# Optimization experiments

Measured on AMD Instinct MI355X. Metric: run time of the kernel, lower is better.

## Reference

```python
import jax, jax.numpy as jnp
import numpy as np

GRID_MIN = -2.0
GRID_MAX = 2.0
NUM_GRIDS = 8
IN_DIM = 512
OUT_DIM = 512
N = 16384
SPLINE_SCALE = 0.1


def setup_inputs() -> dict:
    key = jax.random.key(0)
    k_x, k_sw, k_w, k_b = jax.random.split(key, 4)
    x = jax.random.normal(k_x, (N, IN_DIM), dtype=jnp.float32)
    grid = jnp.linspace(GRID_MIN, GRID_MAX, NUM_GRIDS, dtype=jnp.float32)
    spline_weight = jax.random.normal(k_sw, (IN_DIM * NUM_GRIDS, OUT_DIM), dtype=jnp.float32) * SPLINE_SCALE
    bound = 1.0 / np.sqrt(IN_DIM)
    base_w = jax.random.uniform(k_w, (OUT_DIM, IN_DIM), minval=-bound, maxval=bound, dtype=jnp.float32)
    base_b = jax.random.uniform(k_b, (OUT_DIM,), minval=-bound, maxval=bound, dtype=jnp.float32)
    return {"x": x, "grid": grid, "spline_weight": spline_weight, "base_w": base_w, "base_b": base_b}


def reference(x, grid, spline_weight, base_w, base_b):
    # Gaussian RBF basis over the grid: (N, in_dim, num_grids)
    h = (GRID_MAX - GRID_MIN) / (NUM_GRIDS - 1)  # grid spacing
    basis = jnp.exp(-(((x[..., None] - grid) / h) ** 2))
    ret = basis.reshape(x.shape[0], -1) @ spline_weight  # (N, out_dim)
    base = jax.nn.silu(x) @ base_w.T + base_b
    return ret + base
```

## Files before the change

kernel.cpp:

```cpp
#include <hip/hip_runtime.h>
#include <hip/hip_bf16.h>

typedef __attribute__((ext_vector_type(8))) short short8;
typedef __attribute__((ext_vector_type(4))) float floatx4;

#define N_ROWS   16384
#define IN_DIM   512
#define OUT_DIM  512
#define K_SPLINE 4096
#define K_TOT    4608
#define NPER     36
#define NSPER    32
#define NKTILE   144
#define ROWS_B   128
#define COLS_B   128
#define L2E      1.4426950408889634f
#define C2E      0.13533528323661270f

__device__ __forceinline__ unsigned short f2bf(float f) {
    unsigned int u = __float_as_uint(f);
    unsigned int r = u + 0x7FFFu + ((u >> 16) & 1u);
    return (unsigned short)(r >> 16);
}

__device__ __forceinline__ unsigned packtrunc(float f0, float f1) {
    return __builtin_amdgcn_perm(__float_as_uint(f1), __float_as_uint(f0), 0x07060302);
}

__global__ __launch_bounds__(256) void prep_kernel(
    const float* __restrict__ sw, const float* __restrict__ bw,
    unsigned short* __restrict__ Btf)
{
    const int t     = threadIdx.x;
    const int lane  = t & 63;
    const int kt32  = blockIdx.x * 4 + (t >> 6);
    const int ct    = blockIdx.y;
    const int mn    = lane & 15, q = lane >> 4;
    const int n     = ct * 16 + mn;
    const int kbase = kt32 * 32 + q * 8;
    short8 v;
    if (kbase < K_SPLINE) {
        #pragma unroll
        for (int j = 0; j < 8; ++j)
            v[j] = (short)f2bf(sw[(size_t)(kbase + j) * OUT_DIM + n]);
    } else {
        #pragma unroll
        for (int j = 0; j < 8; ++j)
            v[j] = (short)f2bf(bw[(size_t)n * IN_DIM + (kbase + j - K_SPLINE)]);
    }
    reinterpret_cast<short8*>(Btf)[(size_t)(ct * NKTILE + kt32) * 64 + lane] = v;
}

__device__ __forceinline__ uint4 basis_pack(float X) {
    const float u = fmaf(1.75f, X, 3.5f);
    float b = __builtin_amdgcn_exp2f(-(u * u) * L2E);
    float r = __builtin_amdgcn_exp2f(fmaf(2.0f * L2E, u, -L2E));
    float v[8];
    v[0] = b;
    #pragma unroll
    for (int j = 1; j < 8; ++j) { b *= r; r *= C2E; v[j] = b; }
    uint4 p;
    p.x = packtrunc(v[0], v[1]);
    p.y = packtrunc(v[2], v[3]);
    p.z = packtrunc(v[4], v[5]);
    p.w = packtrunc(v[6], v[7]);
    return p;
}

__device__ __forceinline__ void stageA(unsigned short* arow, const float* xrow,
                                       int rowA, int colq, int p,
                                       float4 xa, float4 xb)
{
    if (p < NSPER) {
        const float xv[8] = {xa.x, xa.y, xa.z, xa.w, xb.x, xb.y, xb.z, xb.w};
        #pragma unroll
        for (int e = 0; e < 8; ++e) {
            const uint4 pk = basis_pack(xv[e]);
            const int blk = (colq * 8 + e) ^ (rowA & 15);
            *reinterpret_cast<uint4*>(arow + blk * 8) = pk;
        }
    } else {
        const float* xs = xrow + (p - NSPER) * 128 + colq * 64;
        #pragma unroll
        for (int e = 0; e < 8; ++e) {
            const float4 a0 = *reinterpret_cast<const float4*>(xs + e * 8);
            const float4 a1 = *reinterpret_cast<const float4*>(xs + e * 8 + 4);
            const float f[8] = {a0.x, a0.y, a0.z, a0.w, a1.x, a1.y, a1.z, a1.w};
            float s[8];
            #pragma unroll
            for (int j = 0; j < 8; ++j)
                s[j] = f[j] * __builtin_amdgcn_rcpf(
                    1.0f + __builtin_amdgcn_exp2f(-f[j] * L2E));
            uint4 pk;
            pk.x = packtrunc(s[0], s[1]);
            pk.y = packtrunc(s[2], s[3]);
            pk.z = packtrunc(s[4], s[5]);
            pk.w = packtrunc(s[6], s[7]);
            const int blk = (colq * 8 + e) ^ (rowA & 15);
            *reinterpret_cast<uint4*>(arow + blk * 8) = pk;
        }
    }
}

template<bool PREP>
__device__ __forceinline__ void load_b(short8 bb[4][2], const short8* __restrict__ Bf,
                                       const size_t* bbase, int p, int kh,
                                       const float* __restrict__ sw,
                                       const float* __restrict__ bw,
                                       int col0, int lane)
{
    if (PREP) {
        #pragma unroll
        for (int nt = 0; nt < 4; ++nt)
            #pragma unroll
            for (int s = 0; s < 2; ++s)
                bb[nt][s] = Bf[bbase[nt] + (size_t)(p * 4 + kh * 2 + s) * 64];
    } else {
        const int mn = lane & 15, q = lane >> 4;
        #pragma unroll
        for (int nt = 0; nt < 4; ++nt) {
            const int n = col0 + nt * 16 + mn;
            #pragma unroll
            for (int s = 0; s < 2; ++s) {
                short8 v;
                #pragma unroll
                for (int j = 0; j < 8; ++j) {
                    const int k = (p * 4 + kh * 2 + s) * 32 + q * 8 + j;
                    const float val = (k < K_SPLINE)
                        ? sw[(size_t)k * OUT_DIM + n]
                        : bw[(size_t)n * IN_DIM + (k - K_SPLINE)];
                    v[j] = (short)f2bf(val);
                }
                bb[nt][s] = v;
            }
        }
    }
}

template<bool PREP>
__global__ __launch_bounds__(256, 2) void kan_kernel(
    const float* __restrict__ x,
    const unsigned short* __restrict__ Btf,
    const float* __restrict__ sw,
    const float* __restrict__ bw,
    const float* __restrict__ bias,
    float* __restrict__ out)
{
    __shared__ unsigned short Als[2][ROWS_B * 128];

    const int tid  = threadIdx.x;
    const int w    = tid >> 6;
    const int lane = tid & 63;
    const int kh   = w >> 1;
    const int wc   = w & 1;
    const int q    = lane >> 4;
    const int mn   = lane & 15;
    const int bid  = blockIdx.x;
    const int row0 = (bid >> 2) * ROWS_B;
    const int col0 = (bid & 3) * COLS_B + wc * 64;

    const int rowA = tid >> 1;
    const int colq = tid & 1;
    const float* xrow = x + (size_t)(row0 + rowA) * IN_DIM;

    size_t bbase[4];
    #pragma unroll
    for (int nt = 0; nt < 4; ++nt)
        bbase[nt] = (size_t)(((col0 >> 4) + nt) * NKTILE) * 64 + lane;
    const short8* Bf = reinterpret_cast<const short8*>(Btf);

    floatx4 acc[8][4];
    #pragma unroll
    for (int i = 0; i < 8; ++i)
        #pragma unroll
        for (int j = 0; j < 4; ++j)
            acc[i][j] = (floatx4){0.f, 0.f, 0.f, 0.f};

    short8 bb[4][2];

    float4 xa = *reinterpret_cast<const float4*>(xrow + colq * 8);
    float4 xb = *reinterpret_cast<const float4*>(xrow + colq * 8 + 4);
    stageA(&Als[0][0] + rowA * 128, xrow, rowA, colq, 0, xa, xb);
    xa = *reinterpret_cast<const float4*>(xrow + 16 + colq * 8);
    xb = *reinterpret_cast<const float4*>(xrow + 16 + colq * 8 + 4);
    __syncthreads();

    for (int p = 0; p < NPER; ++p) {
        const unsigned short* Acur = &Als[p & 1][0];

        load_b<PREP>(bb, Bf, bbase, p, kh, sw, bw, col0, lane);

        if (p + 1 < NPER) {
            stageA(&Als[(p & 1) ^ 1][0] + rowA * 128, xrow, rowA, colq,
                   p + 1, xa, xb);
            if (p + 2 < NSPER) {
                xa = *reinterpret_cast<const float4*>(
                    xrow + (p + 2) * 16 + colq * 8);
                xb = *reinterpret_cast<const float4*>(
                    xrow + (p + 2) * 16 + colq * 8 + 4);
            }
        }

        #pragma unroll
        for (int s = 0; s < 2; ++s) {
            const int st = kh * 2 + s;
            #pragma unroll
            for (int mg = 0; mg < 2; ++mg) {
                short8 af[4];
                #pragma unroll
                for (int mt = 0; mt < 4; ++mt) {
                    const int r = (mg * 4 + mt) * 16 + mn;
                    af[mt] = *reinterpret_cast<const short8*>(
                        Acur + r * 128 + (((st * 4 + q) ^ (r & 15)) * 8));
                }
                __builtin_amdgcn_s_setprio(1);
                #pragma unroll
                for (int mt = 0; mt < 4; ++mt)
                    #pragma unroll
                    for (int nt = 0; nt < 4; ++nt)
                        acc[mg * 4 + mt][nt] = __builtin_amdgcn_mfma_f32_16x16x32_bf16(
                            af[mt], bb[nt][s], acc[mg * 4 + mt][nt], 0, 0, 0);
                __builtin_amdgcn_s_setprio(0);
            }
        }
        __syncthreads();
    }

    floatx4* ex = reinterpret_cast<floatx4*>(&Als[0][0]);
    if (kh) {
        #pragma unroll
        for (int m = 0; m < 4; ++m)
            #pragma unroll
            for (int nt = 0; nt < 4; ++nt)
                ex[((wc * 4 + m) * 4 + nt) * 64 + lane] = acc[m][nt];
    } else {
        #pragma unroll
        for (int m = 0; m < 4; ++m)
            #pragma unroll
            for (int nt = 0; nt < 4; ++nt)
                ex[2048 + ((wc * 4 + m) * 4 + nt) * 64 + lane] = acc[4 + m][nt];
    }
    __syncthreads();
    if (kh) {
        #pragma unroll
        for (int nt = 0; nt < 4; ++nt) {
            const int col = col0 + nt * 16 + mn;
            const float bv = bias[col];
            #pragma unroll
            for (int m = 0; m < 4; ++m) {
                const floatx4 o  = acc[4 + m][nt];
                const floatx4 r2 = ex[2048 + ((wc * 4 + m) * 4 + nt) * 64 + lane];
                const int rb = row0 + (4 + m) * 16 + q * 4;
                #pragma unroll
                for (int e = 0; e < 4; ++e)
                    out[(size_t)(rb + e) * OUT_DIM + col] = o[e] + r2[e] + bv;
            }
        }
    } else {
        #pragma unroll
        for (int nt = 0; nt < 4; ++nt) {
            const int col = col0 + nt * 16 + mn;
            const float bv = bias[col];
            #pragma unroll
            for (int m = 0; m < 4; ++m) {
                const floatx4 o  = acc[m][nt];
                const floatx4 r2 = ex[((wc * 4 + m) * 4 + nt) * 64 + lane];
                const int rb = row0 + m * 16 + q * 4;
                #pragma unroll
                for (int e = 0; e < 4; ++e)
                    out[(size_t)(rb + e) * OUT_DIM + col] = o[e] + r2[e] + bv;
            }
        }
    }
}

extern "C" void kernel_launch(void* const* d_in, const int* in_sizes, int n_in,
                              void* d_out, int out_size, void* d_ws, size_t ws_size,
                              hipStream_t stream)
{
    const float* x    = (const float*)d_in[0];
    const float* sw   = (const float*)d_in[2];
    const float* bw   = (const float*)d_in[3];
    const float* bias = (const float*)d_in[4];
    float* out = (float*)d_out;

    const int nblk = (N_ROWS / ROWS_B) * (OUT_DIM / COLS_B);
    const size_t bt_bytes = (size_t)OUT_DIM * K_TOT * sizeof(unsigned short);
    if (ws_size >= bt_bytes) {
        unsigned short* Btf = (unsigned short*)d_ws;
        prep_kernel<<<dim3(NKTILE / 4, OUT_DIM / 16), 256, 0, stream>>>(sw, bw, Btf);
        kan_kernel<true><<<dim3(nblk), 256, 0, stream>>>(
            x, Btf, sw, bw, bias, out);
    } else {
        kan_kernel<false><<<dim3(nblk), 256, 0, stream>>>(
            x, nullptr, sw, bw, bias, out);
    }
}
```

Baseline: 181.4 us.

## Widen block tile to 256 output columns with 512 threads to share basis staging

Each block now covers 128 rows by 256 output columns using 8 waves instead of 4, split as 4 column waves by 2 K-halves. The Gaussian-basis and SiLU A-tile built in shared memory is therefore reused across twice as many columns, halving the redundant exp and pack work per output. The final split-K reduction through shared memory is reorganised into two phases, so the doubled accumulator exchange still fits in the existing LDS buffer. The cost is fewer blocks, more register pressure from 8 A fragments held at once, and extra barriers in the epilogue.

New measurement: 163.2 us. 10.0% less time.

```diff
diff --git a/kernel.cpp b/kernel.cpp
--- a/kernel.cpp
+++ b/kernel.cpp
@@ -13,7 +13,7 @@
 #define NSPER    32
 #define NKTILE   144
 #define ROWS_B   128
-#define COLS_B   128
+#define COLS_B   256
 #define L2E      1.4426950408889634f
 #define C2E      0.13533528323661270f
 
@@ -67,22 +67,22 @@
     return p;
 }
 
-__device__ __forceinline__ void stageA(unsigned short* arow, const float* xrow,
-                                       int rowA, int colq, int p,
-                                       float4 xa, float4 xb)
-{
+__device__ __forceinline__ void stageA128(unsigned short* dst, const float* xrow,
+                                          int rowA, int colq, int p, float4 xsp)
+{
+    unsigned short* arow = dst + rowA * 128;
     if (p < NSPER) {
-        const float xv[8] = {xa.x, xa.y, xa.z, xa.w, xb.x, xb.y, xb.z, xb.w};
-        #pragma unroll
-        for (int e = 0; e < 8; ++e) {
+        const float xv[4] = {xsp.x, xsp.y, xsp.z, xsp.w};
+        #pragma unroll
+        for (int e = 0; e < 4; ++e) {
             const uint4 pk = basis_pack(xv[e]);
-            const int blk = (colq * 8 + e) ^ (rowA & 15);
+            const int blk = (colq * 4 + e) ^ (rowA & 15);
             *reinterpret_cast<uint4*>(arow + blk * 8) = pk;
         }
     } else {
-        const float* xs = xrow + (p - NSPER) * 128 + colq * 64;
-        #pragma unroll
-        for (int e = 0; e < 8; ++e) {
+        const float* xs = xrow + (p - NSPER) * 128 + colq * 32;
+        #pragma unroll
+        for (int e = 0; e < 4; ++e) {
             const float4 a0 = *reinterpret_cast<const float4*>(xs + e * 8);
             const float4 a1 = *reinterpret_cast<const float4*>(xs + e * 8 + 4);
             const float f[8] = {a0.x, a0.y, a0.z, a0.w, a1.x, a1.y, a1.z, a1.w};
@@ -96,7 +96,7 @@
             pk.y = packtrunc(s[2], s[3]);
             pk.z = packtrunc(s[4], s[5]);
             pk.w = packtrunc(s[6], s[7]);
-            const int blk = (colq * 8 + e) ^ (rowA & 15);
+            const int blk = (colq * 4 + e) ^ (rowA & 15);
             *reinterpret_cast<uint4*>(arow + blk * 8) = pk;
         }
     }
@@ -138,7 +138,7 @@
 }
 
 template<bool PREP>
-__global__ __launch_bounds__(256, 2) void kan_kernel(
+__global__ __launch_bounds__(512, 2) void kan_kernel(
     const float* __restrict__ x,
     const unsigned short* __restrict__ Btf,
     const float* __restrict__ sw,
@@ -151,16 +151,16 @@
     const int tid  = threadIdx.x;
     const int w    = tid >> 6;
     const int lane = tid & 63;
-    const int kh   = w >> 1;
-    const int wc   = w & 1;
+    const int kh   = w >> 2;
+    const int wc   = w & 3;
     const int q    = lane >> 4;
     const int mn   = lane & 15;
     const int bid  = blockIdx.x;
-    const int row0 = (bid >> 2) * ROWS_B;
-    const int col0 = (bid & 3) * COLS_B + wc * 64;
-
-    const int rowA = tid >> 1;
-    const int colq = tid & 1;
+    const int row0 = (bid >> 1) * ROWS_B;
+    const int col0 = (bid & 1) * COLS_B + wc * 64;
+
+    const int rowA = tid >> 2;
+    const int colq = tid & 3;
     const float* xrow = x + (size_t)(row0 + rowA) * IN_DIM;
 
     size_t bbase[4];
@@ -178,11 +178,9 @@
 
     short8 bb[4][2];
 
-    float4 xa = *reinterpret_cast<const float4*>(xrow + colq * 8);
-    float4 xb = *reinterpret_cast<const float4*>(xrow + colq * 8 + 4);
-    stageA(&Als[0][0] + rowA * 128, xrow, rowA, colq, 0, xa, xb);
-    xa = *reinterpret_cast<const float4*>(xrow + 16 + colq * 8);
-    xb = *reinterpret_cast<const float4*>(xrow + 16 + colq * 8 + 4);
+    float4 xsp = *reinterpret_cast<const float4*>(xrow + colq * 4);
+    stageA128(&Als[0][0], xrow, rowA, colq, 0, xsp);
+    xsp = *reinterpret_cast<const float4*>(xrow + 16 + colq * 4);
     __syncthreads();
 
     for (int p = 0; p < NPER; ++p) {
@@ -191,37 +189,30 @@
         load_b<PREP>(bb, Bf, bbase, p, kh, sw, bw, col0, lane);
 
         if (p + 1 < NPER) {
-            stageA(&Als[(p & 1) ^ 1][0] + rowA * 128, xrow, rowA, colq,
-                   p + 1, xa, xb);
-            if (p + 2 < NSPER) {
-                xa = *reinterpret_cast<const float4*>(
-                    xrow + (p + 2) * 16 + colq * 8);
-                xb = *reinterpret_cast<const float4*>(
-                    xrow + (p + 2) * 16 + colq * 8 + 4);
-            }
+            stageA128(&Als[(p & 1) ^ 1][0], xrow, rowA, colq, p + 1, xsp);
+            if (p + 2 < NSPER)
+                xsp = *reinterpret_cast<const float4*>(
+                    xrow + (p + 2) * 16 + colq * 4);
         }
 
         #pragma unroll
         for (int s = 0; s < 2; ++s) {
             const int st = kh * 2 + s;
-            #pragma unroll
-            for (int mg = 0; mg < 2; ++mg) {
-                short8 af[4];
-                #pragma unroll
-                for (int mt = 0; mt < 4; ++mt) {
-                    const int r = (mg * 4 + mt) * 16 + mn;
-                    af[mt] = *reinterpret_cast<const short8*>(
-                        Acur + r * 128 + (((st * 4 + q) ^ (r & 15)) * 8));
-                }
-                __builtin_amdgcn_s_setprio(1);
-                #pragma unroll
-                for (int mt = 0; mt < 4; ++mt)
-                    #pragma unroll
-                    for (int nt = 0; nt < 4; ++nt)
-                        acc[mg * 4 + mt][nt] = __builtin_amdgcn_mfma_f32_16x16x32_bf16(
-                            af[mt], bb[nt][s], acc[mg * 4 + mt][nt], 0, 0, 0);
-                __builtin_amdgcn_s_setprio(0);
-            }
+            short8 af[8];
+            #pragma unroll
+            for (int mt = 0; mt < 8; ++mt) {
+                const int r = mt * 16 + mn;
+                af[mt] = *reinterpret_cast<const short8*>(
+                    Acur + r * 128 + (((st * 4 + q) ^ (r & 15)) * 8));
+            }
+            __builtin_amdgcn_s_setprio(1);
+            #pragma unroll
+            for (int mt = 0; mt < 8; ++mt)
+                #pragma unroll
+                for (int nt = 0; nt < 4; ++nt)
+                    acc[mt][nt] = __builtin_amdgcn_mfma_f32_16x16x32_bf16(
+                        af[mt], bb[nt][s], acc[mt][nt], 0, 0, 0);
+            __builtin_amdgcn_s_setprio(0);
         }
         __syncthreads();
     }
@@ -233,30 +224,9 @@
             #pragma unroll
             for (int nt = 0; nt < 4; ++nt)
                 ex[((wc * 4 + m) * 4 + nt) * 64 + lane] = acc[m][nt];
-    } else {
-        #pragma unroll
-        for (int m = 0; m < 4; ++m)
-            #pragma unroll
-            for (int nt = 0; nt < 4; ++nt)
-                ex[2048 + ((wc * 4 + m) * 4 + nt) * 64 + lane] = acc[4 + m][nt];
-    }
-    __syncthreads();
-    if (kh) {
-        #pragma unroll
-        for (int nt = 0; nt < 4; ++nt) {
-            const int col = col0 + nt * 16 + mn;
-            const float bv = bias[col];
-            #pragma unroll
-            for (int m = 0; m < 4; ++m) {
-                const floatx4 o  = acc[4 + m][nt];
-                const floatx4 r2 = ex[2048 + ((wc * 4 + m) * 4 + nt) * 64 + lane];
-                const int rb = row0 + (4 + m) * 16 + q * 4;
-                #pragma unroll
-                for (int e = 0; e < 4; ++e)
-                    out[(size_t)(rb + e) * OUT_DIM + col] = o[e] + r2[e] + bv;
-            }
-        }
-    } else {
+    }
+    __syncthreads();
+    if (!kh) {
         #pragma unroll
         for (int nt = 0; nt < 4; ++nt) {
             const int col = col0 + nt * 16 + mn;
@@ -266,6 +236,31 @@
                 const floatx4 o  = acc[m][nt];
                 const floatx4 r2 = ex[((wc * 4 + m) * 4 + nt) * 64 + lane];
                 const int rb = row0 + m * 16 + q * 4;
+                #pragma unroll
+                for (int e = 0; e < 4; ++e)
+                    out[(size_t)(rb + e) * OUT_DIM + col] = o[e] + r2[e] + bv;
+            }
+        }
+    }
+    __syncthreads();
+    if (!kh) {
+        #pragma unroll
+        for (int m = 0; m < 4; ++m)
+            #pragma unroll
+            for (int nt = 0; nt < 4; ++nt)
+                ex[((wc * 4 + m) * 4 + nt) * 64 + lane] = acc[4 + m][nt];
+    }
+    __syncthreads();
+    if (kh) {
+        #pragma unroll
+        for (int nt = 0; nt < 4; ++nt) {
+            const int col = col0 + nt * 16 + mn;
+            const float bv = bias[col];
+            #pragma unroll
+            for (int m = 0; m < 4; ++m) {
+                const floatx4 o  = acc[4 + m][nt];
+                const floatx4 r2 = ex[((wc * 4 + m) * 4 + nt) * 64 + lane];
+                const int rb = row0 + (4 + m) * 16 + q * 4;
                 #pragma unroll
                 for (int e = 0; e < 4; ++e)
                     out[(size_t)(rb + e) * OUT_DIM + col] = o[e] + r2[e] + bv;
@@ -289,10 +284,10 @@
     if (ws_size >= bt_bytes) {
         unsigned short* Btf = (unsigned short*)d_ws;
         prep_kernel<<<dim3(NKTILE / 4, OUT_DIM / 16), 256, 0, stream>>>(sw, bw, Btf);
-        kan_kernel<true><<<dim3(nblk), 256, 0, stream>>>(
+        kan_kernel<true><<<dim3(nblk), 512, 0, stream>>>(
             x, Btf, sw, bw, bias, out);
     } else {
-        kan_kernel<false><<<dim3(nblk), 256, 0, stream>>>(
+        kan_kernel<false><<<dim3(nblk), 512, 0, stream>>>(
             x, nullptr, sw, bw, bias, out);
     }
 }
```
